# Kernel tuning notes

Hardware: AMD Instinct MI355X
Metric: run time of the kernel (lower is better)

## Reference

```python
import jax, jax.numpy as jnp
import numpy as np

T, B, I, H = 512, 64, 128, 1024


def setup_inputs() -> dict:
    key = jax.random.key(0)
    k1, k2, k3, k4 = jax.random.split(key, 4)
    # scale recurrent weights to keep tanh in a reasonable regime (spectral-radius-ish)
    return {
        "x": jax.random.normal(k1, (T, B, I), dtype=jnp.float32),
        "h0": jnp.zeros((B, H), dtype=jnp.float32),
        "w_ih": jax.random.normal(k2, (H, I), dtype=jnp.float32) / np.sqrt(I),
        "w_hh": jax.random.normal(k3, (H, H), dtype=jnp.float32) * (0.9 / np.sqrt(H)),
        "b": jax.random.normal(k4, (H,), dtype=jnp.float32) * 0.1,
    }


def reference(x, h0, w_ih, w_hh, b):
    # ESNLayer: python loop over time -> lax.scan with the recurrent carry.
    # cell: h_t = tanh(x_t @ W_ih^T + h_{t-1} @ W_hh^T + b); out_t = h_t
    def step(h, x_t):
        h_new = jnp.tanh(x_t @ w_ih.T + h @ w_hh.T + b)  # [B, H]
        return h_new, h_new

    h_final, outputs = jax.lax.scan(step, h0, x)  # outputs: [T, B, H]
    return outputs, h_final
```

## Files before the change

kernel.cpp:

```cpp
#include <hip/hip_runtime.h>
#include <math.h>


#define T_STEPS 512
#define BATCH   64
#define HDIM    1024
#define IDIM    128
#define KDIM    1152
#define NWG     256
#define NB      8
#define POISON  0x7F7F7F7Fu

typedef float f32x4_t __attribute__((ext_vector_type(4)));

__device__ __forceinline__ void sc_load4x4(const float* p0, const float* p1,
                                           const float* p2, const float* p3,
                                           float4& a, float4& b,
                                           float4& c, float4& d) {
    asm volatile(
        "global_load_dwordx4 %0, %4, off sc0 sc1\n\t"
        "global_load_dwordx4 %1, %5, off sc0 sc1\n\t"
        "global_load_dwordx4 %2, %6, off sc0 sc1\n\t"
        "global_load_dwordx4 %3, %7, off sc0 sc1\n\t"
        "s_waitcnt vmcnt(0)"
        : "=&v"(a), "=&v"(b), "=&v"(c), "=&v"(d)
        : "v"(p0), "v"(p1), "v"(p2), "v"(p3)
        : "memory");
}

__device__ __forceinline__ void sc_store4_nodrain(float* p, float4 v) {
    f32x4_t t;
    t.x = v.x; t.y = v.y; t.z = v.z; t.w = v.w;
    asm volatile("global_store_dwordx4 %0, %1, off sc0 sc1"
                 :: "v"(p), "v"(t) : "memory");
}

__device__ __forceinline__ unsigned chk4(float4 v) {
    return (unsigned)((__float_as_uint(v.x) == POISON) |
                      (__float_as_uint(v.y) == POISON) |
                      (__float_as_uint(v.z) == POISON) |
                      (__float_as_uint(v.w) == POISON));
}

__global__ void transpose_f32(const float* __restrict__ src, float* __restrict__ dst,
                              int R, int C) {
    __shared__ float tile[64][65];
    const int tcol = threadIdx.x & 63;
    const int trow = threadIdx.x >> 6;
    const int nbx = C >> 6;
    const int bx = blockIdx.x % nbx;
    const int by = blockIdx.x / nbx;
    const int c0 = bx << 6, r0 = by << 6;
    for (int i = trow; i < 64; i += 4)
        tile[i][tcol] = src[(size_t)(r0 + i) * C + c0 + tcol];
    __syncthreads();
    for (int i = trow; i < 64; i += 4)
        dst[(size_t)(c0 + i) * R + r0 + tcol] = tile[tcol][i];
}

__global__ __launch_bounds__(512) void esn_persistent(
    const float* __restrict__ x,
    const float* __restrict__ h0,
    const float* __restrict__ WT,
    const float* __restrict__ bias,
    float* __restrict__ out,
    float* __restrict__ hfin)
{
    const int tid  = threadIdx.x;
    const int wg   = blockIdx.x;
    const int wave = tid >> 6;
    const int lane = tid & 63;
    const int jq   = lane & 7;
    const int ksub = lane >> 3;
    const int jblk = ((wg & 7) << 2) | ((wg >> 3) & 3);
    const int bgrp = wg >> 5;
    const int b0   = bgrp << 3;
    const int j0   = (jblk << 5) + (jq << 2);
    const int krec = wave << 7;
    const int kx   = HDIM + (wave << 4) + (ksub << 1);

    __shared__ float  ht2[8 * 1024];
    __shared__ float  htx[8 * 128];
    __shared__ float4 red[2][8 * 8 * 9];

    float4 Wv[18];
    {
        const float* wp = WT + (size_t)krec * HDIM + j0;
        #pragma unroll
        for (int i = 0; i < 4; ++i) {
            const int kk = ((i << 3) + ksub) << 2;
            const float* wk = wp + (size_t)kk * HDIM;
            Wv[i * 4 + 0] = *(const float4*)(wk);
            Wv[i * 4 + 1] = *(const float4*)(wk + HDIM);
            Wv[i * 4 + 2] = *(const float4*)(wk + 2 * HDIM);
            Wv[i * 4 + 3] = *(const float4*)(wk + 3 * HDIM);
        }
        const float* wkx = WT + (size_t)kx * HDIM + j0;
        Wv[16] = *(const float4*)(wkx);
        Wv[17] = *(const float4*)(wkx + HDIM);
    }

    float4 b4 = make_float4(0.f, 0.f, 0.f, 0.f);
    int jj = 0;
    if (lane < 8) {
        jj = (jblk << 5) + (lane << 2);
        b4 = *(const float4*)(bias + jj);
    }

    const int sbb = lane >> 5;
    const int sko = (lane & 31) << 2;
    float* hdst = ht2 + (wave << 10) + (lane << 2);
    const int xr = lane >> 3;
    const int xco = (lane & 7) << 1;
    float* xdst = htx + (wave << 7) + (xr << 4) + xco;
    const float* hb = ht2 + (wave << 10);
    const float* xb = htx + (wave << 7);

    float2 xv2 = *(const float2*)(x + (size_t)(b0 + xr) * IDIM + (wave << 4) + xco);

    for (int t = 0; t < T_STEPS; ++t) {
        *(float2*)xdst = xv2;
        if (t == 0) {
            const float* p = h0 + (size_t)(b0 + sbb) * HDIM + krec + sko;
            *(float4*)(hdst)       = *(const float4*)(p);
            *(float4*)(hdst + 256) = *(const float4*)(p + 2 * HDIM);
            *(float4*)(hdst + 512) = *(const float4*)(p + 4 * HDIM);
            *(float4*)(hdst + 768) = *(const float4*)(p + 6 * HDIM);
        } else {
            const float* p = out + ((size_t)(t - 1) * BATCH + b0 + sbb) * HDIM
                             + krec + sko;
            float4 a, b, c, d;
            do {
                sc_load4x4(p, p + 2 * HDIM, p + 4 * HDIM, p + 6 * HDIM,
                           a, b, c, d);
            } while (__any((int)(chk4(a) | chk4(b) | chk4(c) | chk4(d))));
            *(float4*)(hdst)       = a;
            *(float4*)(hdst + 256) = b;
            *(float4*)(hdst + 512) = c;
            *(float4*)(hdst + 768) = d;
        }

        if (t + 1 < T_STEPS)
            xv2 = *(const float2*)(x + ((size_t)(t + 1) * BATCH + b0 + xr) * IDIM
                                   + (wave << 4) + xco);

        float4 acc[NB];
        #pragma unroll
        for (int bb = 0; bb < NB; ++bb) acc[bb] = make_float4(0.f, 0.f, 0.f, 0.f);

        #pragma unroll
        for (int i = 0; i < 4; ++i) {
            const int ko = ((i << 3) + ksub) << 2;
            const float4 w0 = Wv[i * 4 + 0], w1 = Wv[i * 4 + 1];
            const float4 w2 = Wv[i * 4 + 2], w3 = Wv[i * 4 + 3];
            #pragma unroll
            for (int bb = 0; bb < NB; ++bb) {
                float4 h4 = *(const float4*)(hb + (bb << 7) + ko);
                acc[bb].x = fmaf(w0.x, h4.x, acc[bb].x);
                acc[bb].y = fmaf(w0.y, h4.x, acc[bb].y);
                acc[bb].z = fmaf(w0.z, h4.x, acc[bb].z);
                acc[bb].w = fmaf(w0.w, h4.x, acc[bb].w);
                acc[bb].x = fmaf(w1.x, h4.y, acc[bb].x);
                acc[bb].y = fmaf(w1.y, h4.y, acc[bb].y);
                acc[bb].z = fmaf(w1.z, h4.y, acc[bb].z);
                acc[bb].w = fmaf(w1.w, h4.y, acc[bb].w);
                acc[bb].x = fmaf(w2.x, h4.z, acc[bb].x);
                acc[bb].y = fmaf(w2.y, h4.z, acc[bb].y);
                acc[bb].z = fmaf(w2.z, h4.z, acc[bb].z);
                acc[bb].w = fmaf(w2.w, h4.z, acc[bb].w);
                acc[bb].x = fmaf(w3.x, h4.w, acc[bb].x);
                acc[bb].y = fmaf(w3.y, h4.w, acc[bb].y);
                acc[bb].z = fmaf(w3.z, h4.w, acc[bb].z);
                acc[bb].w = fmaf(w3.w, h4.w, acc[bb].w);
            }
        }
        #pragma unroll
        for (int bb = 0; bb < NB; ++bb) {
            float2 hx = *(const float2*)(xb + (bb << 4) + (ksub << 1));
            acc[bb].x = fmaf(Wv[16].x, hx.x, acc[bb].x);
            acc[bb].y = fmaf(Wv[16].y, hx.x, acc[bb].y);
            acc[bb].z = fmaf(Wv[16].z, hx.x, acc[bb].z);
            acc[bb].w = fmaf(Wv[16].w, hx.x, acc[bb].w);
            acc[bb].x = fmaf(Wv[17].x, hx.y, acc[bb].x);
            acc[bb].y = fmaf(Wv[17].y, hx.y, acc[bb].y);
            acc[bb].z = fmaf(Wv[17].z, hx.y, acc[bb].z);
            acc[bb].w = fmaf(Wv[17].w, hx.y, acc[bb].w);
        }

        #pragma unroll
        for (int bb = 0; bb < NB; ++bb) {
            acc[bb].x += __shfl_xor(acc[bb].x, 8);
            acc[bb].y += __shfl_xor(acc[bb].y, 8);
            acc[bb].z += __shfl_xor(acc[bb].z, 8);
            acc[bb].w += __shfl_xor(acc[bb].w, 8);
            acc[bb].x += __shfl_xor(acc[bb].x, 16);
            acc[bb].y += __shfl_xor(acc[bb].y, 16);
            acc[bb].z += __shfl_xor(acc[bb].z, 16);
            acc[bb].w += __shfl_xor(acc[bb].w, 16);
            acc[bb].x += __shfl_xor(acc[bb].x, 32);
            acc[bb].y += __shfl_xor(acc[bb].y, 32);
            acc[bb].z += __shfl_xor(acc[bb].z, 32);
            acc[bb].w += __shfl_xor(acc[bb].w, 32);
        }
        if (ksub == 0) {
            #pragma unroll
            for (int bb = 0; bb < NB; ++bb)
                red[t & 1][((wave << 3) + jq) * 9 + bb] = acc[bb];
        }
        __syncthreads();

        if (lane < 8) {
            float4 s = make_float4(0.f, 0.f, 0.f, 0.f);
            #pragma unroll
            for (int w = 0; w < 8; ++w) {
                float4 r = red[t & 1][((w << 3) + lane) * 9 + wave];
                s.x += r.x; s.y += r.y; s.z += r.z; s.w += r.w;
            }
            float4 o;
            o.x = tanhf(s.x + b4.x);
            o.y = tanhf(s.y + b4.y);
            o.z = tanhf(s.z + b4.z);
            o.w = tanhf(s.w + b4.w);
            sc_store4_nodrain(out + ((size_t)t * BATCH + b0 + wave) * HDIM + jj, o);
            if (t == T_STEPS - 1)
                *(float4*)(hfin + (size_t)(b0 + wave) * HDIM + jj) = o;
        }
    }
}

extern "C" void kernel_launch(void* const* d_in, const int* in_sizes, int n_in,
                              void* d_out, int out_size, void* d_ws, size_t ws_size,
                              hipStream_t stream) {
    const float* x    = (const float*)d_in[0];
    const float* h0   = (const float*)d_in[1];
    const float* w_ih = (const float*)d_in[2];
    const float* w_hh = (const float*)d_in[3];
    const float* bias = (const float*)d_in[4];
    float* out = (float*)d_out;

    char* ws = (char*)d_ws;
    float* WT = (float*)ws;

    (void)hipMemsetAsync(out, 0x7F,
                         (size_t)T_STEPS * BATCH * HDIM * sizeof(float), stream);
    transpose_f32<<<256, 256, 0, stream>>>(w_hh, WT, HDIM, HDIM);
    transpose_f32<<<32, 256, 0, stream>>>(w_ih, WT + (size_t)HDIM * HDIM, HDIM, IDIM);
    esn_persistent<<<NWG, 512, 0, stream>>>(x, h0, WT, bias,
                                            out, out + (size_t)T_STEPS * BATCH * HDIM);
}
```

Before: 2.767 ms.

## Use packed FMA for recurrent matvec and spread epilogue across 32 lanes

Replaces the scalar FMA chains in the per-step matvec with v_pk_fma_f32 inline asm that uses op_sel to broadcast the h element, so each packed instruction does two FMAs. The epilogue reduction and tanh now run on 32 lanes with one element each, instead of 8 lanes handling four components, and stores become scalar dwords. This targets VALU issue count on the critical serial path of each timestep. In exchange it adds inline asm the compiler cannot schedule around, and more, smaller global stores.

```diff
diff --git a/kernel.cpp b/kernel.cpp
--- a/kernel.cpp
+++ b/kernel.cpp
@@ -12,6 +12,16 @@
 #define POISON  0x7F7F7F7Fu
 
 typedef float f32x4_t __attribute__((ext_vector_type(4)));
+typedef float f32x2_t __attribute__((ext_vector_type(2)));
+
+__device__ __forceinline__ void pk_fma_lo(f32x2_t& d, f32x2_t w, f32x2_t h) {
+    asm("v_pk_fma_f32 %0, %1, %2, %0 op_sel_hi:[1,0,1]"
+        : "+v"(d) : "v"(w), "v"(h));
+}
+__device__ __forceinline__ void pk_fma_hi(f32x2_t& d, f32x2_t w, f32x2_t h) {
+    asm("v_pk_fma_f32 %0, %1, %2, %0 op_sel:[0,1,0]"
+        : "+v"(d) : "v"(w), "v"(h));
+}
 
 __device__ __forceinline__ void sc_load4x4(const float* p0, const float* p1,
                                            const float* p2, const float* p3,
@@ -28,11 +38,9 @@
         : "memory");
 }
 
-__device__ __forceinline__ void sc_store4_nodrain(float* p, float4 v) {
-    f32x4_t t;
-    t.x = v.x; t.y = v.y; t.z = v.z; t.w = v.w;
-    asm volatile("global_store_dwordx4 %0, %1, off sc0 sc1"
-                 :: "v"(p), "v"(t) : "memory");
+__device__ __forceinline__ void sc_store1_nodrain(float* p, float v) {
+    asm volatile("global_store_dword %0, %1, off sc0 sc1"
+                 :: "v"(p), "v"(v) : "memory");
 }
 
 __device__ __forceinline__ unsigned chk4(float4 v) {
@@ -83,29 +91,28 @@
     __shared__ float  htx[8 * 128];
     __shared__ float4 red[2][8 * 8 * 9];
 
-    float4 Wv[18];
+    f32x4_t Wv[18];
     {
         const float* wp = WT + (size_t)krec * HDIM + j0;
         #pragma unroll
         for (int i = 0; i < 4; ++i) {
             const int kk = ((i << 3) + ksub) << 2;
             const float* wk = wp + (size_t)kk * HDIM;
-            Wv[i * 4 + 0] = *(const float4*)(wk);
-            Wv[i * 4 + 1] = *(const float4*)(wk + HDIM);
-            Wv[i * 4 + 2] = *(const float4*)(wk + 2 * HDIM);
-            Wv[i * 4 + 3] = *(const float4*)(wk + 3 * HDIM);
+            Wv[i * 4 + 0] = *(const f32x4_t*)(wk);
+            Wv[i * 4 + 1] = *(const f32x4_t*)(wk + HDIM);
+            Wv[i * 4 + 2] = *(const f32x4_t*)(wk + 2 * HDIM);
+            Wv[i * 4 + 3] = *(const f32x4_t*)(wk + 3 * HDIM);
         }
         const float* wkx = WT + (size_t)kx * HDIM + j0;
-        Wv[16] = *(const float4*)(wkx);
-        Wv[17] = *(const float4*)(wkx + HDIM);
+        Wv[16] = *(const f32x4_t*)(wkx);
+        Wv[17] = *(const f32x4_t*)(wkx + HDIM);
     }
 
-    float4 b4 = make_float4(0.f, 0.f, 0.f, 0.f);
-    int jj = 0;
-    if (lane < 8) {
-        jj = (jblk << 5) + (lane << 2);
-        b4 = *(const float4*)(bias + jj);
-    }
+    const int ejq   = lane & 7;
+    const int ecomp = (lane & 31) >> 3;
+    const int jjs   = (jblk << 5) + (ejq << 2) + ecomp;
+    float bsc = 0.f;
+    if (lane < 32) bsc = bias[jjs];
 
     const int sbb = lane >> 5;
     const int sko = (lane & 31) << 2;
@@ -144,86 +151,73 @@
             xv2 = *(const float2*)(x + ((size_t)(t + 1) * BATCH + b0 + xr) * IDIM
                                    + (wave << 4) + xco);
 
-        float4 acc[NB];
-        #pragma unroll
-        for (int bb = 0; bb < NB; ++bb) acc[bb] = make_float4(0.f, 0.f, 0.f, 0.f);
+        f32x2_t accx[NB], accz[NB];
+        #pragma unroll
+        for (int bb = 0; bb < NB; ++bb) {
+            accx[bb] = (f32x2_t){0.f, 0.f};
+            accz[bb] = (f32x2_t){0.f, 0.f};
+        }
 
         #pragma unroll
         for (int i = 0; i < 4; ++i) {
             const int ko = ((i << 3) + ksub) << 2;
-            const float4 w0 = Wv[i * 4 + 0], w1 = Wv[i * 4 + 1];
-            const float4 w2 = Wv[i * 4 + 2], w3 = Wv[i * 4 + 3];
+            const f32x2_t w0x = Wv[i * 4 + 0].xy, w0z = Wv[i * 4 + 0].zw;
+            const f32x2_t w1x = Wv[i * 4 + 1].xy, w1z = Wv[i * 4 + 1].zw;
+            const f32x2_t w2x = Wv[i * 4 + 2].xy, w2z = Wv[i * 4 + 2].zw;
+            const f32x2_t w3x = Wv[i * 4 + 3].xy, w3z = Wv[i * 4 + 3].zw;
             #pragma unroll
             for (int bb = 0; bb < NB; ++bb) {
-                float4 h4 = *(const float4*)(hb + (bb << 7) + ko);
-                acc[bb].x = fmaf(w0.x, h4.x, acc[bb].x);
-                acc[bb].y = fmaf(w0.y, h4.x, acc[bb].y);
-                acc[bb].z = fmaf(w0.z, h4.x, acc[bb].z);
-                acc[bb].w = fmaf(w0.w, h4.x, acc[bb].w);
-                acc[bb].x = fmaf(w1.x, h4.y, acc[bb].x);
-                acc[bb].y = fmaf(w1.y, h4.y, acc[bb].y);
-                acc[bb].z = fmaf(w1.z, h4.y, acc[bb].z);
-                acc[bb].w = fmaf(w1.w, h4.y, acc[bb].w);
-                acc[bb].x = fmaf(w2.x, h4.z, acc[bb].x);
-                acc[bb].y = fmaf(w2.y, h4.z, acc[bb].y);
-                acc[bb].z = fmaf(w2.z, h4.z, acc[bb].z);
-                acc[bb].w = fmaf(w2.w, h4.z, acc[bb].w);
-                acc[bb].x = fmaf(w3.x, h4.w, acc[bb].x);
-                acc[bb].y = fmaf(w3.y, h4.w, acc[bb].y);
-                acc[bb].z = fmaf(w3.z, h4.w, acc[bb].z);
-                acc[bb].w = fmaf(w3.w, h4.w, acc[bb].w);
+                const f32x4_t h4 = *(const f32x4_t*)(hb + (bb << 7) + ko);
+                const f32x2_t h01 = h4.xy, h23 = h4.zw;
+                pk_fma_lo(accx[bb], w0x, h01);
+                pk_fma_lo(accz[bb], w0z, h01);
+                pk_fma_hi(accx[bb], w1x, h01);
+                pk_fma_hi(accz[bb], w1z, h01);
+                pk_fma_lo(accx[bb], w2x, h23);
+                pk_fma_lo(accz[bb], w2z, h23);
+                pk_fma_hi(accx[bb], w3x, h23);
+                pk_fma_hi(accz[bb], w3z, h23);
             }
         }
+        {
+            const f32x2_t w16x = Wv[16].xy, w16z = Wv[16].zw;
+            const f32x2_t w17x = Wv[17].xy, w17z = Wv[17].zw;
+            #pragma unroll
+            for (int bb = 0; bb < NB; ++bb) {
+                const f32x2_t hx = *(const f32x2_t*)(xb + (bb << 4) + (ksub << 1));
+                pk_fma_lo(accx[bb], w16x, hx);
+                pk_fma_lo(accz[bb], w16z, hx);
+                pk_fma_hi(accx[bb], w17x, hx);
+                pk_fma_hi(accz[bb], w17z, hx);
+            }
+        }
+
         #pragma unroll
         for (int bb = 0; bb < NB; ++bb) {
-            float2 hx = *(const float2*)(xb + (bb << 4) + (ksub << 1));
-            acc[bb].x = fmaf(Wv[16].x, hx.x, acc[bb].x);
-            acc[bb].y = fmaf(Wv[16].y, hx.x, acc[bb].y);
-            acc[bb].z = fmaf(Wv[16].z, hx.x, acc[bb].z);
-            acc[bb].w = fmaf(Wv[16].w, hx.x, acc[bb].w);
-            acc[bb].x = fmaf(Wv[17].x, hx.y, acc[bb].x);
-            acc[bb].y = fmaf(Wv[17].y, hx.y, acc[bb].y);
-            acc[bb].z = fmaf(Wv[17].z, hx.y, acc[bb].z);
-            acc[bb].w = fmaf(Wv[17].w, hx.y, acc[bb].w);
-        }
-
-        #pragma unroll
-        for (int bb = 0; bb < NB; ++bb) {
-            acc[bb].x += __shfl_xor(acc[bb].x, 8);
-            acc[bb].y += __shfl_xor(acc[bb].y, 8);
-            acc[bb].z += __shfl_xor(acc[bb].z, 8);
-            acc[bb].w += __shfl_xor(acc[bb].w, 8);
-            acc[bb].x += __shfl_xor(acc[bb].x, 16);
-            acc[bb].y += __shfl_xor(acc[bb].y, 16);
-            acc[bb].z += __shfl_xor(acc[bb].z, 16);
-            acc[bb].w += __shfl_xor(acc[bb].w, 16);
-            acc[bb].x += __shfl_xor(acc[bb].x, 32);
-            acc[bb].y += __shfl_xor(acc[bb].y, 32);
-            acc[bb].z += __shfl_xor(acc[bb].z, 32);
-            acc[bb].w += __shfl_xor(acc[bb].w, 32);
-        }
-        if (ksub == 0) {
+            float a0 = accx[bb].x, a1 = accx[bb].y;
+            float a2 = accz[bb].x, a3 = accz[bb].y;
+            a0 += __shfl_xor(a0, 8);  a1 += __shfl_xor(a1, 8);
+            a2 += __shfl_xor(a2, 8);  a3 += __shfl_xor(a3, 8);
+            a0 += __shfl_xor(a0, 16); a1 += __shfl_xor(a1, 16);
+            a2 += __shfl_xor(a2, 16); a3 += __shfl_xor(a3, 16);
+            a0 += __shfl_xor(a0, 32); a1 += __shfl_xor(a1, 32);
+            a2 += __shfl_xor(a2, 32); a3 += __shfl_xor(a3, 32);
+            if (ksub == 0)
+                red[t & 1][((wave << 3) + jq) * 9 + bb] =
+                    make_float4(a0, a1, a2, a3);
+        }
+        __syncthreads();
+
+        if (lane < 32) {
+            const float* rp = (const float*)&red[t & 1][0];
+            float s = 0.f;
             #pragma unroll
-            for (int bb = 0; bb < NB; ++bb)
-                red[t & 1][((wave << 3) + jq) * 9 + bb] = acc[bb];
-        }
-        __syncthreads();
-
-        if (lane < 8) {
-            float4 s = make_float4(0.f, 0.f, 0.f, 0.f);
-            #pragma unroll
-            for (int w = 0; w < 8; ++w) {
-                float4 r = red[t & 1][((w << 3) + lane) * 9 + wave];
-                s.x += r.x; s.y += r.y; s.z += r.z; s.w += r.w;
-            }
-            float4 o;
-            o.x = tanhf(s.x + b4.x);
-            o.y = tanhf(s.y + b4.y);
-            o.z = tanhf(s.z + b4.z);
-            o.w = tanhf(s.w + b4.w);
-            sc_store4_nodrain(out + ((size_t)t * BATCH + b0 + wave) * HDIM + jj, o);
+            for (int w = 0; w < 8; ++w)
+                s += rp[(((w << 3) + ejq) * 9 + wave) * 4 + ecomp];
+            const float o = tanhf(s + bsc);
+            sc_store1_nodrain(out + ((size_t)t * BATCH + b0 + wave) * HDIM + jjs, o);
             if (t == T_STEPS - 1)
-                *(float4*)(hfin + (size_t)(b0 + wave) * HDIM + jj) = o;
+                hfin[(size_t)(b0 + wave) * HDIM + jjs] = o;
         }
     }
 }
```

Measured after the change: 2.952 ms. 1.07x slower.

## Split batch across twice as many workgroups, four rows each

Applied to the files above, without the earlier changes.

Doubles the persistent grid from 256 to 512 workgroups, each now handling 4 batch rows instead of 8. This halves the per-step h reload and FMA work per workgroup, cutting per-step latency on the recurrent critical path. In exchange, each workgroup keeps its own full weight slice in registers, so total weight loads double, and more workgroups take part in the flag-polling sync through global memory. All 512 workgroups must be resident at once, or the spin-wait dependency could deadlock.

```diff
diff --git a/kernel.cpp b/kernel.cpp
--- a/kernel.cpp
+++ b/kernel.cpp
@@ -7,24 +7,20 @@
 #define HDIM    1024
 #define IDIM    128
 #define KDIM    1152
-#define NWG     256
-#define NB      8
+#define NWG     512
+#define NB      4
 #define POISON  0x7F7F7F7Fu
 
 typedef float f32x4_t __attribute__((ext_vector_type(4)));
 
-__device__ __forceinline__ void sc_load4x4(const float* p0, const float* p1,
-                                           const float* p2, const float* p3,
-                                           float4& a, float4& b,
-                                           float4& c, float4& d) {
+__device__ __forceinline__ void sc_load2x4(const float* p0, const float* p1,
+                                           float4& a, float4& b) {
     asm volatile(
-        "global_load_dwordx4 %0, %4, off sc0 sc1\n\t"
-        "global_load_dwordx4 %1, %5, off sc0 sc1\n\t"
-        "global_load_dwordx4 %2, %6, off sc0 sc1\n\t"
-        "global_load_dwordx4 %3, %7, off sc0 sc1\n\t"
+        "global_load_dwordx4 %0, %2, off sc0 sc1\n\t"
+        "global_load_dwordx4 %1, %3, off sc0 sc1\n\t"
         "s_waitcnt vmcnt(0)"
-        : "=&v"(a), "=&v"(b), "=&v"(c), "=&v"(d)
-        : "v"(p0), "v"(p1), "v"(p2), "v"(p3)
+        : "=&v"(a), "=&v"(b)
+        : "v"(p0), "v"(p1)
         : "memory");
 }
 
@@ -74,14 +70,14 @@
     const int ksub = lane >> 3;
     const int jblk = ((wg & 7) << 2) | ((wg >> 3) & 3);
     const int bgrp = wg >> 5;
-    const int b0   = bgrp << 3;
+    const int b0   = bgrp << 2;
     const int j0   = (jblk << 5) + (jq << 2);
     const int krec = wave << 7;
     const int kx   = HDIM + (wave << 4) + (ksub << 1);
 
-    __shared__ float  ht2[8 * 1024];
-    __shared__ float  htx[8 * 128];
-    __shared__ float4 red[2][8 * 8 * 9];
+    __shared__ float  ht2[8 * 512];
+    __shared__ float  htx[8 * 64];
+    __shared__ float4 red[2][8 * 8 * 5];
 
     float4 Wv[18];
     {
@@ -109,40 +105,34 @@
 
     const int sbb = lane >> 5;
     const int sko = (lane & 31) << 2;
-    float* hdst = ht2 + (wave << 10) + (lane << 2);
-    const int xr = lane >> 3;
-    const int xco = (lane & 7) << 1;
-    float* xdst = htx + (wave << 7) + (xr << 4) + xco;
-    const float* hb = ht2 + (wave << 10);
-    const float* xb = htx + (wave << 7);
-
-    float2 xv2 = *(const float2*)(x + (size_t)(b0 + xr) * IDIM + (wave << 4) + xco);
+    float* hdst = ht2 + (wave << 9) + (sbb << 7) + sko;
+    const int xr = lane >> 4;
+    const int xco = lane & 15;
+    float* xdst = htx + (wave << 6) + (xr << 4) + xco;
+    const float* hb = ht2 + (wave << 9);
+    const float* xb = htx + (wave << 6);
+
+    float xv = x[(size_t)(b0 + xr) * IDIM + (wave << 4) + xco];
 
     for (int t = 0; t < T_STEPS; ++t) {
-        *(float2*)xdst = xv2;
+        *xdst = xv;
         if (t == 0) {
             const float* p = h0 + (size_t)(b0 + sbb) * HDIM + krec + sko;
             *(float4*)(hdst)       = *(const float4*)(p);
             *(float4*)(hdst + 256) = *(const float4*)(p + 2 * HDIM);
-            *(float4*)(hdst + 512) = *(const float4*)(p + 4 * HDIM);
-            *(float4*)(hdst + 768) = *(const float4*)(p + 6 * HDIM);
         } else {
             const float* p = out + ((size_t)(t - 1) * BATCH + b0 + sbb) * HDIM
                              + krec + sko;
-            float4 a, b, c, d;
+            float4 a, b;
             do {
-                sc_load4x4(p, p + 2 * HDIM, p + 4 * HDIM, p + 6 * HDIM,
-                           a, b, c, d);
-            } while (__any((int)(chk4(a) | chk4(b) | chk4(c) | chk4(d))));
+                sc_load2x4(p, p + 2 * HDIM, a, b);
+            } while (__any((int)(chk4(a) | chk4(b))));
             *(float4*)(hdst)       = a;
             *(float4*)(hdst + 256) = b;
-            *(float4*)(hdst + 512) = c;
-            *(float4*)(hdst + 768) = d;
         }
 
         if (t + 1 < T_STEPS)
-            xv2 = *(const float2*)(x + ((size_t)(t + 1) * BATCH + b0 + xr) * IDIM
-                                   + (wave << 4) + xco);
+            xv = x[((size_t)(t + 1) * BATCH + b0 + xr) * IDIM + (wave << 4) + xco];
 
         float4 acc[NB];
         #pragma unroll
@@ -205,15 +195,15 @@
         if (ksub == 0) {
             #pragma unroll
             for (int bb = 0; bb < NB; ++bb)
-                red[t & 1][((wave << 3) + jq) * 9 + bb] = acc[bb];
+                red[t & 1][((wave << 3) + jq) * 5 + bb] = acc[bb];
         }
         __syncthreads();
 
-        if (lane < 8) {
+        if (wave < 4 && lane < 8) {
             float4 s = make_float4(0.f, 0.f, 0.f, 0.f);
             #pragma unroll
             for (int w = 0; w < 8; ++w) {
-                float4 r = red[t & 1][((w << 3) + lane) * 9 + wave];
+                float4 r = red[t & 1][((w << 3) + lane) * 5 + wave];
                 s.x += r.x; s.y += r.y; s.z += r.z; s.w += r.w;
             }
             float4 o;
```

Measured after the change: 3.816 ms. 1.38x slower.
